# Optimization experiments

Measured on AMD Instinct MI355X. Metric: run time of the kernel, lower is better.

The kernel has to match this reference:

```python
import jax, jax.numpy as jnp
import numpy as np

N_NODES = 100000


def setup_inputs() -> dict:
    key = jax.random.key(0)
    k1, k2, k3, k4, k5 = jax.random.split(key, 5)
    in_dim, out_dim, n_edges = 128, 128, 640000
    x = jax.random.normal(k1, (N_NODES, in_dim), dtype=jnp.float32)
    src = jax.random.randint(k2, (n_edges,), 0, N_NODES, dtype=jnp.int32)
    dst = jax.random.randint(k3, (n_edges,), 0, N_NODES, dtype=jnp.int32)
    edge_index = jnp.stack([src, dst], axis=0)  # [2, E]
    # nn.Linear default init: U(-1/sqrt(in_dim), 1/sqrt(in_dim))
    bound = 1.0 / np.sqrt(in_dim)
    W = jax.random.uniform(k4, (out_dim, in_dim), minval=-bound, maxval=bound, dtype=jnp.float32)
    b = jax.random.uniform(k5, (out_dim,), minval=-bound, maxval=bound, dtype=jnp.float32)
    return {"x": x, "edge_index": edge_index, "W": W, "b": b}


def reference(x, edge_index, W, b):
    src, dst = edge_index[0], edge_index[1]
    # scatter-sum of gathered source features into destination nodes
    agg = jax.ops.segment_sum(x[src], dst, num_segments=N_NODES)       # [N, d]
    deg = jax.ops.segment_sum(jnp.ones((src.shape[0], 1), x.dtype), dst,
                              num_segments=N_NODES)                     # [N, 1]
    deg = jnp.maximum(deg, 1.0)
    h = agg / deg + x                                                   # mean-agg + residual
    out = jax.nn.relu(h @ W.T + b)                                      # linear + relu (dropout p=0)
    return out
```

## Files before the change

### kernel.cpp

```cpp
#include <hip/hip_runtime.h>
#include <hip/hip_bf16.h>

constexpr int N_NODES = 100000;
constexpr int DIM     = 128;
constexpr int N_EDGES = 640000;

constexpr int CHUNK     = 1024;
constexpr int N_CHUNKS  = (N_NODES + CHUNK - 1) / CHUNK;
constexpr int BINCAP    = 8192;
constexpr int EPB       = 1024;
constexpr int SRC_BITS  = 17;
constexpr int SRC_MASK  = (1 << SRC_BITS) - 1;

constexpr int YNB         = 32;
constexpr int GEMM_BLOCKS = N_NODES / YNB;
constexpr int BIN_BLOCKS  = N_EDGES / EPB;
constexpr int DSTRIDE     = 640;

typedef __attribute__((ext_vector_type(4))) float        f32x4;
typedef __attribute__((ext_vector_type(8))) short        bf16x8;
typedef __attribute__((ext_vector_type(4))) unsigned int u32x4;

static __device__ inline unsigned short f2bf(float f) {
    __hip_bfloat16 h = __float2bfloat16(f);
    return *reinterpret_cast<unsigned short*>(&h);
}
static __device__ inline float bf_lo(unsigned u) { return __uint_as_float(u << 16); }
static __device__ inline float bf_hi(unsigned u) { return __uint_as_float(u & 0xffff0000u); }

static __device__ inline bf16x8 pack8(f32x4 a, f32x4 b) {
    bf16x8 v;
    v[0] = (short)f2bf(a.x); v[1] = (short)f2bf(a.y);
    v[2] = (short)f2bf(a.z); v[3] = (short)f2bf(a.w);
    v[4] = (short)f2bf(b.x); v[5] = (short)f2bf(b.y);
    v[6] = (short)f2bf(b.z); v[7] = (short)f2bf(b.w);
    return v;
}

__global__ __launch_bounds__(256) void gcn_gemm_bin(
    const float* __restrict__ x,
    const float* __restrict__ W,
    const int* __restrict__ esrc,
    const int* __restrict__ edst,
    unsigned short* __restrict__ y,
    unsigned int* __restrict__ blkdata,
    int* __restrict__ bcnt,
    int* __restrict__ bst)
{
    __shared__ unsigned short wl[DIM][DIM + 8];
    __shared__ int bh[N_CHUNKS];
    __shared__ int bpre[128];

    const int tid = threadIdx.x;

    if (blockIdx.x >= GEMM_BLOCKS) {
        const int b  = blockIdx.x - GEMM_BLOCKS;
        const int e0 = b * EPB + tid * 4;

        if (tid < N_CHUNKS) bh[tid] = 0;
        __syncthreads();

        const int4 s4 = *reinterpret_cast<const int4*>(esrc + e0);
        const int4 d4 = *reinterpret_cast<const int4*>(edst + e0);
        const int ds[4] = {d4.x, d4.y, d4.z, d4.w};
        const int ss[4] = {s4.x, s4.y, s4.z, s4.w};

        int bin[4], pos[4];
        unsigned pv[4];
        #pragma unroll
        for (int q = 0; q < 4; ++q) {
            bin[q] = ds[q] >> 10;
            pv[q]  = (unsigned)ss[q] | ((unsigned)(ds[q] & (CHUNK - 1)) << SRC_BITS);
            pos[q] = atomicAdd(&bh[bin[q]], 1);
        }
        __syncthreads();

        if (tid < 128) bpre[tid] = (tid < N_CHUNKS) ? bh[tid] : 0;
        __syncthreads();
        for (int d = 1; d < 128; d <<= 1) {
            int add = 0;
            if (tid < 128 && tid >= d) add = bpre[tid - d];
            __syncthreads();
            if (tid < 128) bpre[tid] += add;
            __syncthreads();
        }
        if (tid < N_CHUNKS) {
            bcnt[tid * DSTRIDE + b] = bh[tid];
            bst [tid * DSTRIDE + b] = (tid > 0) ? bpre[tid - 1] : 0;
        }
        __syncthreads();

        #pragma unroll
        for (int q = 0; q < 4; ++q) {
            const int excl = (bin[q] > 0) ? bpre[bin[q] - 1] : 0;
            blkdata[(size_t)b * EPB + excl + pos[q]] = pv[q];
        }
        return;
    }

    const int n0 = blockIdx.x * YNB;

    #pragma unroll
    for (int rep = 0; rep < 8; ++rep) {
        const int e   = rep * 2048 + tid * 8;
        const int row = e >> 7;
        const int col = e & 127;
        f32x4 a = *reinterpret_cast<const f32x4*>(W + e);
        f32x4 b = *reinterpret_cast<const f32x4*>(W + e + 4);
        *reinterpret_cast<bf16x8*>(&wl[row][col]) = pack8(a, b);
    }
    __syncthreads();

    const int w    = tid >> 6;
    const int lane = tid & 63;
    const int r    = lane & 15;
    const int g    = lane >> 4;
    const int rowt  = w & 1;
    const int cbase = 4 * (w >> 1);

    bf16x8 af[4];
    #pragma unroll
    for (int t = 0; t < 4; ++t) {
        const float* xp = x + (size_t)(n0 + 16 * rowt + r) * DIM + 32 * t + 8 * g;
        f32x4 a = *reinterpret_cast<const f32x4*>(xp);
        f32x4 b = *reinterpret_cast<const f32x4*>(xp + 4);
        af[t] = pack8(a, b);
    }

    #pragma unroll
    for (int cc = 0; cc < 4; ++cc) {
        const int c = cbase + cc;
        f32x4 acc = {0.f, 0.f, 0.f, 0.f};
        #pragma unroll
        for (int t = 0; t < 4; ++t) {
            bf16x8 wf = *reinterpret_cast<const bf16x8*>(&wl[16 * c + r][32 * t + 8 * g]);
            acc = __builtin_amdgcn_mfma_f32_16x16x32_bf16(af[t], wf, acc, 0, 0, 0);
        }
        #pragma unroll
        for (int q = 0; q < 4; ++q)
            y[(size_t)(n0 + 16 * rowt + 4 * g + q) * DIM + 16 * c + r] =
                f2bf(acc[q]);
    }
}

__global__ __launch_bounds__(256) void gcn_build(
    const unsigned int* __restrict__ blkdata,
    const int* __restrict__ bcnt,
    const int* __restrict__ bst,
    unsigned int* __restrict__ csr,
    int* __restrict__ off)
{
    __shared__ unsigned stage[BINCAP];
    __shared__ int hist[CHUNK];
    __shared__ int s[256];

    const int c = blockIdx.x;
    const int t = threadIdx.x;

    #pragma unroll
    for (int q = 0; q < 4; ++q) hist[t + 256 * q] = 0;

    const int base = t * 3;
    int v0 = (base + 0 < BIN_BLOCKS) ? bcnt[c * DSTRIDE + base + 0] : 0;
    int v1 = (base + 1 < BIN_BLOCKS) ? bcnt[c * DSTRIDE + base + 1] : 0;
    int v2 = (base + 2 < BIN_BLOCKS) ? bcnt[c * DSTRIDE + base + 2] : 0;

    s[t] = v0 + v1 + v2;
    __syncthreads();
    for (int d = 1; d < 256; d <<= 1) {
        int add = (t >= d) ? s[t - d] : 0;
        __syncthreads();
        s[t] += add;
        __syncthreads();
    }
    const int nb   = min(s[255], BINCAP);
    const int excl = (t > 0) ? s[t - 1] : 0;

    {
        int run = excl;
        const int vv[3] = {v0, v1, v2};
        #pragma unroll
        for (int k = 0; k < 3; ++k) {
            const int i = base + k;
            const int n = vv[k];
            if (i < BIN_BLOCKS && n > 0) {
                const unsigned* p = blkdata + (size_t)i * EPB + bst[c * DSTRIDE + i];
                for (int e = 0; e < n; ++e)
                    if (run + e < BINCAP) stage[run + e] = p[e];
                run += n;
            }
        }
    }
    __syncthreads();

    for (int e = t; e < nb; e += 256)
        atomicAdd(&hist[stage[e] >> SRC_BITS], 1);
    __syncthreads();

    int h0 = hist[4 * t + 0], h1 = hist[4 * t + 1];
    int h2 = hist[4 * t + 2], h3 = hist[4 * t + 3];
    s[t] = h0 + h1 + h2 + h3;
    __syncthreads();
    for (int d = 1; d < 256; d <<= 1) {
        int add = (t >= d) ? s[t - d] : 0;
        __syncthreads();
        s[t] += add;
        __syncthreads();
    }
    int nexcl = (t > 0) ? s[t - 1] : 0;

    const int st0 = nexcl;
    const int st1 = nexcl + h0;
    const int st2 = nexcl + h0 + h1;
    const int st3 = nexcl + h0 + h1 + h2;
    hist[4 * t + 0] = st0;  hist[4 * t + 1] = st1;
    hist[4 * t + 2] = st2;  hist[4 * t + 3] = st3;

    const int nbase = c * CHUNK;
    if (nbase + 4 * t + 0 < N_NODES) off[nbase + 4 * t + 0] = st0 | (h0 << 13);
    if (nbase + 4 * t + 1 < N_NODES) off[nbase + 4 * t + 1] = st1 | (h1 << 13);
    if (nbase + 4 * t + 2 < N_NODES) off[nbase + 4 * t + 2] = st2 | (h2 << 13);
    if (nbase + 4 * t + 3 < N_NODES) off[nbase + 4 * t + 3] = st3 | (h3 << 13);
    __syncthreads();

    for (int e = t; e < nb; e += 256) {
        unsigned v = stage[e];
        int slot   = atomicAdd(&hist[v >> SRC_BITS], 1);
        csr[(size_t)c * BINCAP + slot] = v & SRC_MASK;
    }
}

static __device__ inline void acc8(float* acc, u32x4 v) {
    #pragma unroll
    for (int q = 0; q < 4; ++q) {
        unsigned u = v[q];
        acc[2 * q]     += bf_lo(u);
        acc[2 * q + 1] += bf_hi(u);
    }
}

__global__ __launch_bounds__(256) void gcn_agg(
    const unsigned short* __restrict__ y,
    const int* __restrict__ off,
    const unsigned int* __restrict__ csr,
    const float* __restrict__ bias,
    float* __restrict__ out)
{
    const int tid    = threadIdx.x;
    const int lane16 = tid & 15;
    const int n      = blockIdx.x * 16 + (tid >> 4);
    const int col8   = lane16 * 8;

    const int meta  = off[n];
    const int count = meta >> 13;
    int i           = (n >> 10) * BINCAP + (meta & (BINCAP - 1));
    const int end   = i + count;

    float acc[8];
    #pragma unroll
    for (int q = 0; q < 8; ++q) acc[q] = 0.0f;

    for (; i + 4 <= end; i += 4) {
        int s0 = csr[i], s1 = csr[i + 1], s2 = csr[i + 2], s3 = csr[i + 3];
        u32x4 v0 = *reinterpret_cast<const u32x4*>(y + (size_t)s0 * DIM + col8);
        u32x4 v1 = *reinterpret_cast<const u32x4*>(y + (size_t)s1 * DIM + col8);
        u32x4 v2 = *reinterpret_cast<const u32x4*>(y + (size_t)s2 * DIM + col8);
        u32x4 v3 = *reinterpret_cast<const u32x4*>(y + (size_t)s3 * DIM + col8);
        acc8(acc, v0); acc8(acc, v1); acc8(acc, v2); acc8(acc, v3);
    }
    for (; i < end; ++i) {
        u32x4 v = *reinterpret_cast<const u32x4*>(y + (size_t)csr[i] * DIM + col8);
        acc8(acc, v);
    }

    const float inv = 1.0f / fmaxf((float)count, 1.0f);
    const u32x4 yr = *reinterpret_cast<const u32x4*>(y + (size_t)n * DIM + col8);
    const f32x4 b0 = *reinterpret_cast<const f32x4*>(bias + col8);
    const f32x4 b1 = *reinterpret_cast<const f32x4*>(bias + col8 + 4);

    f32x4 o0, o1;
    o0.x = fmaxf(acc[0] * inv + bf_lo(yr[0]) + b0.x, 0.0f);
    o0.y = fmaxf(acc[1] * inv + bf_hi(yr[0]) + b0.y, 0.0f);
    o0.z = fmaxf(acc[2] * inv + bf_lo(yr[1]) + b0.z, 0.0f);
    o0.w = fmaxf(acc[3] * inv + bf_hi(yr[1]) + b0.w, 0.0f);
    o1.x = fmaxf(acc[4] * inv + bf_lo(yr[2]) + b1.x, 0.0f);
    o1.y = fmaxf(acc[5] * inv + bf_hi(yr[2]) + b1.y, 0.0f);
    o1.z = fmaxf(acc[6] * inv + bf_lo(yr[3]) + b1.z, 0.0f);
    o1.w = fmaxf(acc[7] * inv + bf_hi(yr[3]) + b1.w, 0.0f);

    __builtin_nontemporal_store(o0, reinterpret_cast<f32x4*>(out + (size_t)n * DIM + col8));
    __builtin_nontemporal_store(o1, reinterpret_cast<f32x4*>(out + (size_t)n * DIM + col8 + 4));
}

extern "C" void kernel_launch(void* const* d_in, const int* in_sizes, int n_in,
                              void* d_out, int out_size, void* d_ws, size_t ws_size,
                              hipStream_t stream)
{
    const float* x    = (const float*)d_in[0];
    const int*   eidx = (const int*)d_in[1];
    const float* W    = (const float*)d_in[2];
    const float* bias = (const float*)d_in[3];
    float*       out  = (float*)d_out;

    const int* esrc = eidx;
    const int* edst = eidx + N_EDGES;

    int* bcnt             = (int*)d_ws;
    int* bst              = bcnt + N_CHUNKS * DSTRIDE;
    unsigned int* blkdata = (unsigned int*)(bst + N_CHUNKS * DSTRIDE);
    unsigned int* csr     = blkdata + (size_t)BIN_BLOCKS * EPB;
    int* off              = (int*)(csr + (size_t)N_CHUNKS * BINCAP);
    unsigned short* y     = (unsigned short*)(off + 100352);

    gcn_gemm_bin<<<GEMM_BLOCKS + BIN_BLOCKS, 256, 0, stream>>>(
        x, W, esrc, edst, y, blkdata, bcnt, bst);
    gcn_build<<<N_CHUNKS, 256, 0, stream>>>(blkdata, bcnt, bst, csr, off);
    gcn_agg  <<<N_NODES / 16, 256, 0, stream>>>(y, off, csr, bias, out);
}
```

Before: 91.95 us.

## Pad CSR rows to multiples of four with self-indices and parallelize staging gather

Each destination's CSR segment is padded to a multiple of four using the node's own index, so the aggregation loop can use 128-bit index loads with no scalar tail. The extra self contributions are cancelled by scaling the residual term. The build kernel now fills the stage buffer by binary search over per-block prefix offsets, replacing serial per-thread copies, and some input loads are marked nontemporal. In exchange, CSR storage and the offset bit packing grow, and the aggregation does extra gathers of the node's own row.

Measured after the change: 109.6 us. 1.19x slower.

```diff
diff --git a/kernel.cpp b/kernel.cpp
--- a/kernel.cpp
+++ b/kernel.cpp
@@ -8,6 +8,7 @@
 constexpr int CHUNK     = 1024;
 constexpr int N_CHUNKS  = (N_NODES + CHUNK - 1) / CHUNK;
 constexpr int BINCAP    = 8192;
+constexpr int CSRCAP    = 12288;
 constexpr int EPB       = 1024;
 constexpr int SRC_BITS  = 17;
 constexpr int SRC_MASK  = (1 << SRC_BITS) - 1;
@@ -20,6 +21,7 @@
 typedef __attribute__((ext_vector_type(4))) float        f32x4;
 typedef __attribute__((ext_vector_type(8))) short        bf16x8;
 typedef __attribute__((ext_vector_type(4))) unsigned int u32x4;
+typedef __attribute__((ext_vector_type(4))) int          i32x4;
 
 static __device__ inline unsigned short f2bf(float f) {
     __hip_bfloat16 h = __float2bfloat16(f);
@@ -60,8 +62,10 @@
         if (tid < N_CHUNKS) bh[tid] = 0;
         __syncthreads();
 
-        const int4 s4 = *reinterpret_cast<const int4*>(esrc + e0);
-        const int4 d4 = *reinterpret_cast<const int4*>(edst + e0);
+        const i32x4 s4 = __builtin_nontemporal_load(
+            reinterpret_cast<const i32x4*>(esrc + e0));
+        const i32x4 d4 = __builtin_nontemporal_load(
+            reinterpret_cast<const i32x4*>(edst + e0));
         const int ds[4] = {d4.x, d4.y, d4.z, d4.w};
         const int ss[4] = {s4.x, s4.y, s4.z, s4.w};
 
@@ -122,8 +126,8 @@
     #pragma unroll
     for (int t = 0; t < 4; ++t) {
         const float* xp = x + (size_t)(n0 + 16 * rowt + r) * DIM + 32 * t + 8 * g;
-        f32x4 a = *reinterpret_cast<const f32x4*>(xp);
-        f32x4 b = *reinterpret_cast<const f32x4*>(xp + 4);
+        f32x4 a = __builtin_nontemporal_load(reinterpret_cast<const f32x4*>(xp));
+        f32x4 b = __builtin_nontemporal_load(reinterpret_cast<const f32x4*>(xp) + 1);
         af[t] = pack8(a, b);
     }
 
@@ -153,6 +157,8 @@
     __shared__ unsigned stage[BINCAP];
     __shared__ int hist[CHUNK];
     __shared__ int s[256];
+    __shared__ int rpre[BIN_BLOCKS];
+    __shared__ int rbase[BIN_BLOCKS];
 
     const int c = blockIdx.x;
     const int t = threadIdx.x;
@@ -176,20 +182,27 @@
     const int nb   = min(s[255], BINCAP);
     const int excl = (t > 0) ? s[t - 1] : 0;
 
-    {
-        int run = excl;
-        const int vv[3] = {v0, v1, v2};
-        #pragma unroll
-        for (int k = 0; k < 3; ++k) {
-            const int i = base + k;
-            const int n = vv[k];
-            if (i < BIN_BLOCKS && n > 0) {
-                const unsigned* p = blkdata + (size_t)i * EPB + bst[c * DSTRIDE + i];
-                for (int e = 0; e < n; ++e)
-                    if (run + e < BINCAP) stage[run + e] = p[e];
-                run += n;
-            }
-        }
+    if (base + 0 < BIN_BLOCKS) {
+        rpre [base + 0] = excl;
+        rbase[base + 0] = (base + 0) * EPB + bst[c * DSTRIDE + base + 0];
+    }
+    if (base + 1 < BIN_BLOCKS) {
+        rpre [base + 1] = excl + v0;
+        rbase[base + 1] = (base + 1) * EPB + bst[c * DSTRIDE + base + 1];
+    }
+    if (base + 2 < BIN_BLOCKS) {
+        rpre [base + 2] = excl + v0 + v1;
+        rbase[base + 2] = (base + 2) * EPB + bst[c * DSTRIDE + base + 2];
+    }
+    __syncthreads();
+
+    for (int e = t; e < nb; e += 256) {
+        int lo = 0, hi = BIN_BLOCKS - 1;
+        while (lo < hi) {
+            int mid = (lo + hi + 1) >> 1;
+            if (rpre[mid] <= e) lo = mid; else hi = mid - 1;
+        }
+        stage[e] = blkdata[rbase[lo] + (e - rpre[lo])];
     }
     __syncthreads();
 
@@ -197,9 +210,12 @@
         atomicAdd(&hist[stage[e] >> SRC_BITS], 1);
     __syncthreads();
 
-    int h0 = hist[4 * t + 0], h1 = hist[4 * t + 1];
-    int h2 = hist[4 * t + 2], h3 = hist[4 * t + 3];
-    s[t] = h0 + h1 + h2 + h3;
+    const int h0 = hist[4 * t + 0], h1 = hist[4 * t + 1];
+    const int h2 = hist[4 * t + 2], h3 = hist[4 * t + 3];
+    const int p0 = (h0 + 3) & ~3, p1 = (h1 + 3) & ~3;
+    const int p2 = (h2 + 3) & ~3, p3 = (h3 + 3) & ~3;
+
+    s[t] = p0 + p1 + p2 + p3;
     __syncthreads();
     for (int d = 1; d < 256; d <<= 1) {
         int add = (t >= d) ? s[t - d] : 0;
@@ -207,26 +223,39 @@
         s[t] += add;
         __syncthreads();
     }
-    int nexcl = (t > 0) ? s[t - 1] : 0;
+    const int nexcl = (t > 0) ? s[t - 1] : 0;
 
     const int st0 = nexcl;
-    const int st1 = nexcl + h0;
-    const int st2 = nexcl + h0 + h1;
-    const int st3 = nexcl + h0 + h1 + h2;
+    const int st1 = st0 + p0;
+    const int st2 = st1 + p1;
+    const int st3 = st2 + p2;
     hist[4 * t + 0] = st0;  hist[4 * t + 1] = st1;
     hist[4 * t + 2] = st2;  hist[4 * t + 3] = st3;
 
     const int nbase = c * CHUNK;
-    if (nbase + 4 * t + 0 < N_NODES) off[nbase + 4 * t + 0] = st0 | (h0 << 13);
-    if (nbase + 4 * t + 1 < N_NODES) off[nbase + 4 * t + 1] = st1 | (h1 << 13);
-    if (nbase + 4 * t + 2 < N_NODES) off[nbase + 4 * t + 2] = st2 | (h2 << 13);
-    if (nbase + 4 * t + 3 < N_NODES) off[nbase + 4 * t + 3] = st3 | (h3 << 13);
-    __syncthreads();
-
+    if (nbase + 4 * t + 0 < N_NODES) off[nbase + 4 * t + 0] = st0 | (h0 << 14);
+    if (nbase + 4 * t + 1 < N_NODES) off[nbase + 4 * t + 1] = st1 | (h1 << 14);
+    if (nbase + 4 * t + 2 < N_NODES) off[nbase + 4 * t + 2] = st2 | (h2 << 14);
+    if (nbase + 4 * t + 3 < N_NODES) off[nbase + 4 * t + 3] = st3 | (h3 << 14);
+    __syncthreads();
+
+    unsigned int* creg = csr + (size_t)c * CSRCAP;
     for (int e = t; e < nb; e += 256) {
         unsigned v = stage[e];
         int slot   = atomicAdd(&hist[v >> SRC_BITS], 1);
-        csr[(size_t)c * BINCAP + slot] = v & SRC_MASK;
+        creg[slot] = v & SRC_MASK;
+    }
+
+    {
+        const int sts[4] = {st0, st1, st2, st3};
+        const int hs[4]  = {h0, h1, h2, h3};
+        const int ps[4]  = {p0, p1, p2, p3};
+        #pragma unroll
+        for (int j = 0; j < 4; ++j) {
+            const unsigned gn = (unsigned)(nbase + 4 * t + j);
+            for (int k = sts[j] + hs[j]; k < sts[j] + ps[j]; ++k)
+                creg[k] = gn;
+        }
     }
 }
 
@@ -251,42 +280,40 @@
     const int n      = blockIdx.x * 16 + (tid >> 4);
     const int col8   = lane16 * 8;
 
-    const int meta  = off[n];
-    const int count = meta >> 13;
-    int i           = (n >> 10) * BINCAP + (meta & (BINCAP - 1));
-    const int end   = i + count;
+    const int meta   = off[n];
+    const int count  = meta >> 14;
+    const int start  = (n >> 10) * CSRCAP + (meta & 16383);
+    const int padded = (count + 3) & ~3;
+    const int end    = start + padded;
 
     float acc[8];
     #pragma unroll
     for (int q = 0; q < 8; ++q) acc[q] = 0.0f;
 
-    for (; i + 4 <= end; i += 4) {
-        int s0 = csr[i], s1 = csr[i + 1], s2 = csr[i + 2], s3 = csr[i + 3];
-        u32x4 v0 = *reinterpret_cast<const u32x4*>(y + (size_t)s0 * DIM + col8);
-        u32x4 v1 = *reinterpret_cast<const u32x4*>(y + (size_t)s1 * DIM + col8);
-        u32x4 v2 = *reinterpret_cast<const u32x4*>(y + (size_t)s2 * DIM + col8);
-        u32x4 v3 = *reinterpret_cast<const u32x4*>(y + (size_t)s3 * DIM + col8);
+    for (int i = start; i < end; i += 4) {
+        const i32x4 i4 = *reinterpret_cast<const i32x4*>(csr + i);
+        u32x4 v0 = *reinterpret_cast<const u32x4*>(y + (size_t)i4.x * DIM + col8);
+        u32x4 v1 = *reinterpret_cast<const u32x4*>(y + (size_t)i4.y * DIM + col8);
+        u32x4 v2 = *reinterpret_cast<const u32x4*>(y + (size_t)i4.z * DIM + col8);
+        u32x4 v3 = *reinterpret_cast<const u32x4*>(y + (size_t)i4.w * DIM + col8);
         acc8(acc, v0); acc8(acc, v1); acc8(acc, v2); acc8(acc, v3);
     }
-    for (; i < end; ++i) {
-        u32x4 v = *reinterpret_cast<const u32x4*>(y + (size_t)csr[i] * DIM + col8);
-        acc8(acc, v);
-    }
-
-    const float inv = 1.0f / fmaxf((float)count, 1.0f);
+
+    const float inv    = 1.0f / fmaxf((float)count, 1.0f);
+    const float yscale = 1.0f - (float)(padded - count) * inv;
     const u32x4 yr = *reinterpret_cast<const u32x4*>(y + (size_t)n * DIM + col8);
     const f32x4 b0 = *reinterpret_cast<const f32x4*>(bias + col8);
     const f32x4 b1 = *reinterpret_cast<const f32x4*>(bias + col8 + 4);
 
     f32x4 o0, o1;
-    o0.x = fmaxf(acc[0] * inv + bf_lo(yr[0]) + b0.x, 0.0f);
-    o0.y = fmaxf(acc[1] * inv + bf_hi(yr[0]) + b0.y, 0.0f);
-    o0.z = fmaxf(acc[2] * inv + bf_lo(yr[1]) + b0.z, 0.0f);
-    o0.w = fmaxf(acc[3] * inv + bf_hi(yr[1]) + b0.w, 0.0f);
-    o1.x = fmaxf(acc[4] * inv + bf_lo(yr[2]) + b1.x, 0.0f);
-    o1.y = fmaxf(acc[5] * inv + bf_hi(yr[2]) + b1.y, 0.0f);
-    o1.z = fmaxf(acc[6] * inv + bf_lo(yr[3]) + b1.z, 0.0f);
-    o1.w = fmaxf(acc[7] * inv + bf_hi(yr[3]) + b1.w, 0.0f);
+    o0.x = fmaxf(acc[0] * inv + yscale * bf_lo(yr[0]) + b0.x, 0.0f);
+    o0.y = fmaxf(acc[1] * inv + yscale * bf_hi(yr[0]) + b0.y, 0.0f);
+    o0.z = fmaxf(acc[2] * inv + yscale * bf_lo(yr[1]) + b0.z, 0.0f);
+    o0.w = fmaxf(acc[3] * inv + yscale * bf_hi(yr[1]) + b0.w, 0.0f);
+    o1.x = fmaxf(acc[4] * inv + yscale * bf_lo(yr[2]) + b1.x, 0.0f);
+    o1.y = fmaxf(acc[5] * inv + yscale * bf_hi(yr[2]) + b1.y, 0.0f);
+    o1.z = fmaxf(acc[6] * inv + yscale * bf_lo(yr[3]) + b1.z, 0.0f);
+    o1.w = fmaxf(acc[7] * inv + yscale * bf_hi(yr[3]) + b1.w, 0.0f);
 
     __builtin_nontemporal_store(o0, reinterpret_cast<f32x4*>(out + (size_t)n * DIM + col8));
     __builtin_nontemporal_store(o1, reinterpret_cast<f32x4*>(out + (size_t)n * DIM + col8 + 4));
@@ -309,7 +336,7 @@
     int* bst              = bcnt + N_CHUNKS * DSTRIDE;
     unsigned int* blkdata = (unsigned int*)(bst + N_CHUNKS * DSTRIDE);
     unsigned int* csr     = blkdata + (size_t)BIN_BLOCKS * EPB;
-    int* off              = (int*)(csr + (size_t)N_CHUNKS * BINCAP);
+    int* off              = (int*)(csr + (size_t)N_CHUNKS * CSRCAP);
     unsigned short* y     = (unsigned short*)(off + 100352);
 
     gcn_gemm_bin<<<GEMM_BLOCKS + BIN_BLOCKS, 256, 0, stream>>>(
```
